# Kernel optimization log

Measured on AMD Instinct MI355X. Metric: run time of the kernel, lower is better.

Reference implementation:

```python
import jax, jax.numpy as jnp
import numpy as np

NMODELS, SZ_IN, SZ_OUT, B = 128, 256, 256, 4096

def setup_inputs() -> dict:
    key = jax.random.key(0)
    k1, k2, k3, k4 = jax.random.split(key, 4)
    inp = jax.random.normal(k1, (B, SZ_IN), dtype=jnp.float32)
    agent_ids = jax.random.randint(k2, (B,), 0, NMODELS, dtype=jnp.int32)
    # Embedding tables (init ~ N(0,1) like nn.Embedding default)
    weight_lut = jax.random.normal(k3, (NMODELS, SZ_IN * SZ_OUT), dtype=jnp.float32)
    bias_lut = jax.random.normal(k4, (NMODELS, SZ_OUT), dtype=jnp.float32)
    return {"inp": inp, "agent_ids": agent_ids, "weight_lut": weight_lut, "bias_lut": bias_lut}

def reference(inp, agent_ids, weight_lut, bias_lut):
    # per-id weight gather -> [B, sz_in, sz_out]
    W = weight_lut[agent_ids].reshape(-1, SZ_IN, SZ_OUT)
    b = bias_lut[agent_ids]  # [B, sz_out]
    out = jnp.einsum('bi,bio->bo', inp, W) + b
    return out
```

## Files before the change

kernel.cpp:

```cpp
#include <hip/hip_runtime.h>

#define NMODELS 128
#define SZ_IN 256
#define SZ_OUT 256
#define CHUNK 16
#define MAXLIST 192
#define LDSK 264
#define NT 512
#define FRAGSTRIDE 520

typedef __attribute__((ext_vector_type(4))) float f32x4;
typedef __attribute__((ext_vector_type(8))) short bf16x8;
typedef __attribute__((ext_vector_type(4))) short s16x4;

__device__ __forceinline__ short f2bf(float f) {
  union { float f; unsigned u; } v;
  v.f = f;
  const unsigned r = v.u + 0x7FFFu + ((v.u >> 16) & 1u);
  return (short)(r >> 16);
}

__global__ __launch_bounds__(NT, 2) void linmulti_final(
    const float* __restrict__ inp, const int* __restrict__ ids,
    const float* __restrict__ wlut, const float* __restrict__ blut,
    float* __restrict__ out, int B) {
  const int ch = blockIdx.x;
  const int m = blockIdx.y;
  const int tid = threadIdx.x;
  const int lane = tid & 63;
  const int wv = tid >> 6;
  const int q = lane >> 4;
  const int n16 = lane & 15;
  const int col = ch * 128 + wv * 16 + n16;

  __shared__ short Wfrag[64 * FRAGSTRIDE];
  __shared__ int list[MAXLIST];
  __shared__ int wcnt[8][8];
  short* As = Wfrag;

  int myid[8];
#pragma unroll
  for (int v = 0; v < 8; ++v) {
    const int b = v * NT + tid;
    myid[v] = (b < B) ? ids[b] : -1;
  }

  const float* __restrict__ Wb = wlut + (size_t)m * (SZ_IN * SZ_OUT) + ch * 128;
  f32x4 wraw[16];
#pragma unroll
  for (int v = 0; v < 16; ++v) {
    const int e4 = v * NT + tid;
    const int r = e4 >> 5;
    const int c4 = e4 & 31;
    wraw[v] = *(const f32x4*)(Wb + (size_t)r * SZ_OUT + c4 * 4);
  }

#pragma unroll
  for (int v = 0; v < 8; ++v) {
    const unsigned long long mk = __ballot(myid[v] == m);
    if (lane == 0) wcnt[v][wv] = __popcll(mk);
  }
  __syncthreads();
  int run = 0;
#pragma unroll
  for (int v = 0; v < 8; ++v) {
    int wbase = run;
    for (int w = 0; w < wv; ++w) wbase += wcnt[v][w];
    const unsigned long long mk = __ballot(myid[v] == m);
    if (myid[v] == m) {
      const int p = wbase + __popcll(mk & ((1ULL << lane) - 1ULL));
      if (p < MAXLIST) list[p] = v * NT + tid;
    }
    for (int w = 0; w < 8; ++w) run += wcnt[v][w];
  }

#pragma unroll
  for (int v = 0; v < 16; ++v) {
    const int e4 = v * NT + tid;
    const int r = e4 >> 5;
    const int c0 = (e4 & 31) * 4;
    const int kb = r >> 5;
    const int qq = (r >> 3) & 3;
    const int jj = r & 7;
#pragma unroll
    for (int e = 0; e < 4; ++e) {
      const int c = c0 + e;
      Wfrag[(kb * 8 + (c >> 4)) * FRAGSTRIDE + ((qq * 16) + (c & 15)) * 8 + jj] =
          f2bf(wraw[v][e]);
    }
  }
  __syncthreads();

  bf16x8 bfr[8];
#pragma unroll
  for (int kb = 0; kb < 8; ++kb)
    bfr[kb] = *(const bf16x8*)(Wfrag + (kb * 8 + wv) * FRAGSTRIDE + lane * 8);
  __syncthreads();

  const int cnt = (run < MAXLIST) ? run : MAXLIST;
  if (cnt == 0) return;

  const float bias_c = blut[m * SZ_OUT + col];

  const int nchunk = (cnt + CHUNK - 1) / CHUNK;
  for (int c = 0; c < nchunk; ++c) {
    const int s0 = c * CHUNK;
    if (c) __syncthreads();
#pragma unroll
    for (int v = 0; v < 2; ++v) {
      const int e4 = v * NT + tid;
      const int s = e4 >> 6, f4 = e4 & 63;
      int p = s0 + s;
      if (p > cnt - 1) p = cnt - 1;
      const f32x4 a = ((const f32x4*)(inp + (size_t)list[p] * SZ_IN))[f4];
      s16x4 h;
#pragma unroll
      for (int j = 0; j < 4; ++j) h[j] = f2bf(a[j]);
      *(s16x4*)(As + s * LDSK + f4 * 4) = h;
    }
    __syncthreads();

    f32x4 acc = (f32x4){0.f, 0.f, 0.f, 0.f};
#pragma unroll
    for (int kb = 0; kb < 8; ++kb) {
      const bf16x8 afr = *(const bf16x8*)(As + n16 * LDSK + kb * 32 + q * 8);
      acc = __builtin_amdgcn_mfma_f32_16x16x32_bf16(afr, bfr[kb], acc, 0, 0, 0);
    }

#pragma unroll
    for (int r = 0; r < 4; ++r) {
      const int srow = q * 4 + r;
      if (s0 + srow < cnt)
        out[(size_t)list[s0 + srow] * SZ_OUT + col] = acc[r] + bias_c;
    }
  }
}

extern "C" void kernel_launch(void* const* d_in, const int* in_sizes, int n_in,
                              void* d_out, int out_size, void* d_ws, size_t ws_size,
                              hipStream_t stream) {
  const float* inp = (const float*)d_in[0];
  const int* ids = (const int*)d_in[1];
  const float* wlut = (const float*)d_in[2];
  const float* blut = (const float*)d_in[3];
  float* out = (float*)d_out;
  const int B = in_sizes[1];

  linmulti_final<<<dim3(2, NMODELS), NT, 0, stream>>>(inp, ids, wlut, blut, out, B);
}
```

Measured before the change: 87.38 us.

## Split columns into 64-wide blocks, batch 64 rows per stage, atomic list build

Each block now owns 64 output columns instead of 128, so the grid grows to 4x128 blocks and the launch bound allows 4 blocks per CU. Input rows are loaded for up to 64 selected samples at once into a separate LDS buffer, and two wave groups split the 16-row MFMA chunks between them. This cuts the number of barriers per chunk. The ballot and prefix-sum list construction is replaced by a shared atomic counter, which makes the order of list entries nondeterministic but leaves results unchanged. Each block now repeats the id scan and input-row reads for half as many columns, so those loads are duplicated across more blocks.

```diff
diff --git a/kernel.cpp b/kernel.cpp
--- a/kernel.cpp
+++ b/kernel.cpp
@@ -3,11 +3,13 @@
 #define NMODELS 128
 #define SZ_IN 256
 #define SZ_OUT 256
-#define CHUNK 16
 #define MAXLIST 192
 #define LDSK 264
 #define NT 512
 #define FRAGSTRIDE 520
+#define CPB 64
+#define NTILES 4
+#define AROWS 64
 
 typedef __attribute__((ext_vector_type(4))) float f32x4;
 typedef __attribute__((ext_vector_type(8))) short bf16x8;
@@ -20,7 +22,7 @@
   return (short)(r >> 16);
 }
 
-__global__ __launch_bounds__(NT, 2) void linmulti_final(
+__global__ __launch_bounds__(NT, 4) void linmulti_v13(
     const float* __restrict__ inp, const int* __restrict__ ids,
     const float* __restrict__ wlut, const float* __restrict__ blut,
     float* __restrict__ out, int B) {
@@ -29,14 +31,18 @@
   const int tid = threadIdx.x;
   const int lane = tid & 63;
   const int wv = tid >> 6;
+  const int nt = wv & 3;
+  const int par = wv >> 2;
   const int q = lane >> 4;
   const int n16 = lane & 15;
-  const int col = ch * 128 + wv * 16 + n16;
+  const int col = ch * CPB + nt * 16 + n16;
 
-  __shared__ short Wfrag[64 * FRAGSTRIDE];
+  __shared__ short Wfrag[32 * FRAGSTRIDE];
+  __shared__ short As[AROWS * LDSK];
   __shared__ int list[MAXLIST];
-  __shared__ int wcnt[8][8];
-  short* As = Wfrag;
+  __shared__ int cnt0;
+
+  if (tid == 0) cnt0 = 0;
 
   int myid[8];
 #pragma unroll
@@ -45,47 +51,52 @@
     myid[v] = (b < B) ? ids[b] : -1;
   }
 
-  const float* __restrict__ Wb = wlut + (size_t)m * (SZ_IN * SZ_OUT) + ch * 128;
-  f32x4 wraw[16];
+  const float* __restrict__ Wb = wlut + (size_t)m * (SZ_IN * SZ_OUT) + ch * CPB;
+  f32x4 wraw[8];
 #pragma unroll
-  for (int v = 0; v < 16; ++v) {
+  for (int v = 0; v < 8; ++v) {
     const int e4 = v * NT + tid;
-    const int r = e4 >> 5;
-    const int c4 = e4 & 31;
+    const int r = e4 >> 4;
+    const int c4 = e4 & 15;
     wraw[v] = *(const f32x4*)(Wb + (size_t)r * SZ_OUT + c4 * 4);
+  }
+
+  __syncthreads();
+
+#pragma unroll
+  for (int v = 0; v < 8; ++v) {
+    if (myid[v] == m) {
+      const int p = atomicAdd(&cnt0, 1);
+      if (p < MAXLIST) list[p] = v * NT + tid;
+    }
+  }
+  __syncthreads();
+  const int cnt = (cnt0 < MAXLIST) ? cnt0 : MAXLIST;
+  if (cnt == 0) return;
+
+  f32x4 araw[8];
+#pragma unroll
+  for (int v = 0; v < 8; ++v) {
+    const int e4 = v * NT + tid;
+    const int s = e4 >> 6;
+    const int f4 = e4 & 63;
+    int p = s;
+    if (p > cnt - 1) p = cnt - 1;
+    araw[v] = ((const f32x4*)(inp + (size_t)list[p] * SZ_IN))[f4];
   }
 
 #pragma unroll
   for (int v = 0; v < 8; ++v) {
-    const unsigned long long mk = __ballot(myid[v] == m);
-    if (lane == 0) wcnt[v][wv] = __popcll(mk);
-  }
-  __syncthreads();
-  int run = 0;
-#pragma unroll
-  for (int v = 0; v < 8; ++v) {
-    int wbase = run;
-    for (int w = 0; w < wv; ++w) wbase += wcnt[v][w];
-    const unsigned long long mk = __ballot(myid[v] == m);
-    if (myid[v] == m) {
-      const int p = wbase + __popcll(mk & ((1ULL << lane) - 1ULL));
-      if (p < MAXLIST) list[p] = v * NT + tid;
-    }
-    for (int w = 0; w < 8; ++w) run += wcnt[v][w];
-  }
-
-#pragma unroll
-  for (int v = 0; v < 16; ++v) {
     const int e4 = v * NT + tid;
-    const int r = e4 >> 5;
-    const int c0 = (e4 & 31) * 4;
+    const int r = e4 >> 4;
+    const int c0 = (e4 & 15) * 4;
     const int kb = r >> 5;
     const int qq = (r >> 3) & 3;
     const int jj = r & 7;
 #pragma unroll
     for (int e = 0; e < 4; ++e) {
       const int c = c0 + e;
-      Wfrag[(kb * 8 + (c >> 4)) * FRAGSTRIDE + ((qq * 16) + (c & 15)) * 8 + jj] =
+      Wfrag[(kb * NTILES + (c >> 4)) * FRAGSTRIDE + ((qq * 16) + (c & 15)) * 8 + jj] =
           f2bf(wraw[v][e]);
     }
   }
@@ -94,44 +105,52 @@
   bf16x8 bfr[8];
 #pragma unroll
   for (int kb = 0; kb < 8; ++kb)
-    bfr[kb] = *(const bf16x8*)(Wfrag + (kb * 8 + wv) * FRAGSTRIDE + lane * 8);
-  __syncthreads();
-
-  const int cnt = (run < MAXLIST) ? run : MAXLIST;
-  if (cnt == 0) return;
+    bfr[kb] = *(const bf16x8*)(Wfrag + (kb * NTILES + nt) * FRAGSTRIDE + lane * 8);
 
   const float bias_c = blut[m * SZ_OUT + col];
 
-  const int nchunk = (cnt + CHUNK - 1) / CHUNK;
-  for (int c = 0; c < nchunk; ++c) {
-    const int s0 = c * CHUNK;
-    if (c) __syncthreads();
+  for (int base = 0;;) {
 #pragma unroll
-    for (int v = 0; v < 2; ++v) {
+    for (int v = 0; v < 8; ++v) {
       const int e4 = v * NT + tid;
-      const int s = e4 >> 6, f4 = e4 & 63;
-      int p = s0 + s;
-      if (p > cnt - 1) p = cnt - 1;
-      const f32x4 a = ((const f32x4*)(inp + (size_t)list[p] * SZ_IN))[f4];
+      const int s = e4 >> 6;
+      const int f4 = e4 & 63;
       s16x4 h;
 #pragma unroll
-      for (int j = 0; j < 4; ++j) h[j] = f2bf(a[j]);
+      for (int j = 0; j < 4; ++j) h[j] = f2bf(araw[v][j]);
       *(s16x4*)(As + s * LDSK + f4 * 4) = h;
     }
     __syncthreads();
 
-    f32x4 acc = (f32x4){0.f, 0.f, 0.f, 0.f};
+    const int rows = ((cnt - base) < AROWS) ? (cnt - base) : AROWS;
+    const int nchunk = (rows + 15) >> 4;
+    for (int c = par; c < nchunk; c += 2) {
+      f32x4 acc = (f32x4){0.f, 0.f, 0.f, 0.f};
 #pragma unroll
-    for (int kb = 0; kb < 8; ++kb) {
-      const bf16x8 afr = *(const bf16x8*)(As + n16 * LDSK + kb * 32 + q * 8);
-      acc = __builtin_amdgcn_mfma_f32_16x16x32_bf16(afr, bfr[kb], acc, 0, 0, 0);
+      for (int kb = 0; kb < 8; ++kb) {
+        const bf16x8 afr =
+            *(const bf16x8*)(As + (c * 16 + n16) * LDSK + kb * 32 + q * 8);
+        acc = __builtin_amdgcn_mfma_f32_16x16x32_bf16(afr, bfr[kb], acc, 0, 0, 0);
+      }
+#pragma unroll
+      for (int r = 0; r < 4; ++r) {
+        const int gr = base + c * 16 + q * 4 + r;
+        if (gr < cnt)
+          out[(size_t)list[gr] * SZ_OUT + col] = acc[r] + bias_c;
+      }
     }
 
+    base += AROWS;
+    if (base >= cnt) break;
+    __syncthreads();
 #pragma unroll
-    for (int r = 0; r < 4; ++r) {
-      const int srow = q * 4 + r;
-      if (s0 + srow < cnt)
-        out[(size_t)list[s0 + srow] * SZ_OUT + col] = acc[r] + bias_c;
+    for (int v = 0; v < 8; ++v) {
+      const int e4 = v * NT + tid;
+      const int s = e4 >> 6;
+      const int f4 = e4 & 63;
+      int p = base + s;
+      if (p > cnt - 1) p = cnt - 1;
+      araw[v] = ((const f32x4*)(inp + (size_t)list[p] * SZ_IN))[f4];
     }
   }
 }
@@ -146,5 +165,5 @@
   float* out = (float*)d_out;
   const int B = in_sizes[1];
 
-  linmulti_final<<<dim3(2, NMODELS), NT, 0, stream>>>(inp, ids, wlut, blut, out, B);
+  linmulti_v13<<<dim3(4, NMODELS), NT, 0, stream>>>(inp, ids, wlut, blut, out, B);
 }
```

New measurement: 84.68 us. 3.1% less time.
